# Performance work log

Measured on AMD Instinct MI355X. Metric: run time of the kernel, lower is better.

The kernel has to match this reference:

```python
import jax, jax.numpy as jnp
import numpy as np

B, N, K = 4, 512, 10
PI_SCALE = 0.05  # keeps sum_k pi in (0, 0.5) so the [1e-8, 1] clamp does not saturate at 1
MCMC_KEY = jax.random.key(42)


def setup_inputs() -> dict:
    key = jax.random.key(0)
    k1, k2, k3, k4 = jax.random.split(key, 4)
    mu = jax.random.normal(k1, (B, N, K), dtype=jnp.float32)
    sig = jax.random.uniform(k2, (B, N, K), dtype=jnp.float32)
    pi = jax.random.uniform(k3, (B, N, K), dtype=jnp.float32) * PI_SCALE
    A_0 = jax.random.uniform(k4, (N, N), dtype=jnp.float32)
    return {"mu": mu, "sig": sig, "pi": pi, "A_0": A_0, "num_samples": 100}


def reference(mu, sig, pi, A_0, num_samples):
    b, n, k = mu.shape

    # Mixture-weighted proposal mean/std:  sum_k softmax(pi)_k * {mu,sig}_k
    component_probs = jax.nn.softmax(pi, axis=-1)          # [B,N,K]
    selected_mu = jnp.sum(component_probs * mu, axis=-1)    # [B,N]
    selected_sig = jnp.sum(component_probs * sig, axis=-1)  # [B,N]

    # edge_probs[b,i,j] = clamp(sum_k pi[b,i,k]) -- constant in j; hoisted out of the loop
    # since it depends only on pi (the torch code recomputes it every step).
    edge_probs = jnp.clip(jnp.sum(pi, axis=2), 1e-8, 1.0)[:, :, None]  # [B,N,1]
    log_ep = jnp.log(edge_probs)                                        # [B,N,1]
    log_1mep = jnp.log(1.0 - edge_probs)                                # [B,N,1]

    def log_likelihood(A):  # A: [B,N,N] -> [N]  (sum over dims 0,1 as in torch)
        return jnp.sum(A * log_ep + (1.0 - A) * log_1mep, axis=(0, 1))

    def step(carry, t):
        current_A, acc = carry
        kk = jax.random.fold_in(MCMC_KEY, t)
        k_noise, k_unif = jax.random.split(kk)
        noise = jax.random.normal(k_noise, (b, n), dtype=selected_mu.dtype)
        proposed_mu = selected_mu + noise * selected_sig              # [B,N]
        # sigmoid of rank-1 outer product: einsum('bnc,bmc->bnm') with c==1
        proposed_A = jax.nn.sigmoid(proposed_mu[:, :, None] * proposed_mu[:, None, :])
        ratio = jnp.mean(jnp.clip(jnp.exp(log_likelihood(proposed_A) - log_likelihood(current_A)), 0.0, 1.0))
        accept = jax.random.uniform(k_unif, (b,)) < ratio             # [B] bool
        current_A = jnp.where(accept[:, None, None], proposed_A, current_A)
        return (current_A, acc + current_A), None

    cur0 = jnp.broadcast_to(A_0, (b, n, n)).astype(mu.dtype)
    acc0 = jnp.zeros((b, n, n), dtype=mu.dtype)
    (_, acc), _ = jax.lax.scan(step, (cur0, acc0), jnp.arange(num_samples))
    return acc / num_samples
```

## Files before the change

### kernel.cpp

```cpp
#include <hip/hip_runtime.h>
#include <stdint.h>

#define T_STEPS 100
#define BB 4
#define NN 512
#define KK 10
#define TBTOT (T_STEPS * BB)
#define LLT_ELT ((size_t)TBTOT * NN)

typedef float f4 __attribute__((ext_vector_type(4)));

__device__ __forceinline__ uint32_t rotl32(uint32_t v, int d) {
  return (v << d) | (v >> (32 - d));
}

__device__ __forceinline__ void tf2x32(uint32_t k0, uint32_t k1,
                                       uint32_t& x0, uint32_t& x1) {
  uint32_t k2 = k0 ^ k1 ^ 0x1BD11BDAu;
  x0 += k0; x1 += k1;
#define TFR(r) { x0 += x1; x1 = rotl32(x1, r); x1 ^= x0; }
  TFR(13) TFR(15) TFR(26) TFR(6)   x0 += k1; x1 += k2 + 1u;
  TFR(17) TFR(29) TFR(16) TFR(24)  x0 += k2; x1 += k0 + 2u;
  TFR(13) TFR(15) TFR(26) TFR(6)   x0 += k0; x1 += k1 + 3u;
  TFR(17) TFR(29) TFR(16) TFR(24)  x0 += k1; x1 += k2 + 4u;
  TFR(13) TFR(15) TFR(26) TFR(6)   x0 += k2; x1 += k0 + 5u;
#undef TFR
}

__device__ __forceinline__ float bits_to_u01(uint32_t bits) {
  return __fsub_rn(__uint_as_float((bits >> 9) | 0x3f800000u), 1.0f);
}

__device__ __forceinline__ float erfinv_f32(float x) {
  float w = -logf(__fmul_rn(__fsub_rn(1.0f, x), __fadd_rn(1.0f, x)));
  float p;
  if (w < 5.0f) {
    w = __fsub_rn(w, 2.5f);
    p = 2.81022636e-08f;
    p = __fadd_rn(__fmul_rn(p, w), 3.43273939e-07f);
    p = __fadd_rn(__fmul_rn(p, w), -3.5233877e-06f);
    p = __fadd_rn(__fmul_rn(p, w), -4.39150654e-06f);
    p = __fadd_rn(__fmul_rn(p, w), 0.00021858087f);
    p = __fadd_rn(__fmul_rn(p, w), -0.00125372503f);
    p = __fadd_rn(__fmul_rn(p, w), -0.00417768164f);
    p = __fadd_rn(__fmul_rn(p, w), 0.246640727f);
    p = __fadd_rn(__fmul_rn(p, w), 1.50140941f);
  } else {
    w = __fsub_rn(sqrtf(w), 3.0f);
    p = -0.000200214257f;
    p = __fadd_rn(__fmul_rn(p, w), 0.000100950558f);
    p = __fadd_rn(__fmul_rn(p, w), 0.00134934322f);
    p = __fadd_rn(__fmul_rn(p, w), -0.00367342844f);
    p = __fadd_rn(__fmul_rn(p, w), 0.00573950773f);
    p = __fadd_rn(__fmul_rn(p, w), -0.0076224613f);
    p = __fadd_rn(__fmul_rn(p, w), 0.00943887047f);
    p = __fadd_rn(__fmul_rn(p, w), 1.00167406f);
    p = __fadd_rn(__fmul_rn(p, w), 2.83297682f);
  }
  return __fmul_rn(p, x);
}

__device__ __forceinline__ float fast_sigmoid(float x) {
  float e = __expf(-x);
  return __builtin_amdgcn_rcpf(__fadd_rn(1.0f, e));
}

template <int CTRL>
__device__ __forceinline__ float dpp_add(float x) {
  int v = __builtin_amdgcn_update_dpp(0, __float_as_int(x), CTRL, 0xF, 0xF, true);
  return __fadd_rn(x, __int_as_float(v));
}
__device__ __forceinline__ float readlane_f(float x, int lane) {
  return __int_as_float(__builtin_amdgcn_readlane(__float_as_int(x), lane));
}

__global__ void prep_kernel(const float* __restrict__ mu,
                            const float* __restrict__ sig,
                            const float* __restrict__ pi,
                            float* __restrict__ sm, float* __restrict__ ss,
                            float* __restrict__ Lf) {
  int m = blockIdx.x * blockDim.x + threadIdx.x;
  if (m >= BB * NN) return;
  const float* pp = pi + m * KK;
  float mx = pp[0];
  for (int k = 1; k < KK; k++) mx = fmaxf(mx, pp[k]);
  float e[KK]; float s = 0.0f;
  for (int k = 0; k < KK; k++) { e[k] = expf(__fsub_rn(pp[k], mx)); s = __fadd_rn(s, e[k]); }
  float smv = 0.0f, ssv = 0.0f, eps = 0.0f;
  for (int k = 0; k < KK; k++) {
    float p = e[k] / s;
    smv = __fadd_rn(smv, __fmul_rn(p, mu[m * KK + k]));
    ssv = __fadd_rn(ssv, __fmul_rn(p, sig[m * KK + k]));
    eps = __fadd_rn(eps, pp[k]);
  }
  sm[m] = smv; ss[m] = ssv;
  float ep = fminf(fmaxf(eps, 1e-8f), 1.0f);
  float lep = logf(ep);
  float l1 = logf(__fsub_rn(1.0f, ep));
  Lf[m] = (float)((double)lep - (double)l1);
}

__global__ void rng_kernel(const float* __restrict__ sm,
                           const float* __restrict__ ss,
                           float* __restrict__ pm, float* __restrict__ uacc) {
  int id = blockIdx.x * blockDim.x + threadIdx.x;
  if (id >= T_STEPS * BB * NN) return;
  int t = id >> 11;
  int m = id & 2047;

  uint32_t kk0 = 0u, kk1 = (uint32_t)t;
  tf2x32(0u, 42u, kk0, kk1);
  uint32_t n0 = 0u, n1 = 0u; tf2x32(kk0, kk1, n0, n1);
  uint32_t y0 = 0u, y1 = (uint32_t)m;
  tf2x32(n0, n1, y0, y1);
  uint32_t bits = y0 ^ y1;

  float u01 = bits_to_u01(bits);
  const float lo = -0.99999994f;
  float u = fmaxf(lo, __fadd_rn(__fmul_rn(u01, 2.0f), lo));
  float z = __fmul_rn(1.41421356237309515f, erfinv_f32(u));
  pm[id] = __fadd_rn(sm[m], __fmul_rn(z, ss[m]));

  if (m < 4) {
    uint32_t u0 = 0u, u1 = 1u; tf2x32(kk0, kk1, u0, u1);
    uint32_t c0 = 0u, c1 = (uint32_t)m;
    tf2x32(u0, u1, c0, c1);
    uacc[t * 4 + m] = bits_to_u01(c0 ^ c1);
  }
}

template <int SPLIT>
__global__ __launch_bounds__(512) void ll_kernel(const float* __restrict__ pm,
                                                 const float* __restrict__ Lf,
                                                 const float* __restrict__ A0,
                                                 float* __restrict__ llt_p,
                                                 float* __restrict__ ll0_p) {
  constexpr int CH = NN / SPLIT;
  __shared__ float spm[CH];
  __shared__ float sLc[CH];
  int j = threadIdx.x;
  int bi = blockIdx.x;
  if (bi < TBTOT * SPLIT) {
    int tb = bi / SPLIT;
    int s = bi - tb * SPLIT;
    int b = tb & 3;
    int i0 = s * CH;
    if (j < CH) {
      spm[j] = pm[tb * NN + i0 + j];
      sLc[j] = Lf[b * NN + i0 + j];
    }
    float pmj = pm[tb * NN + j];
    __syncthreads();
    double acc = 0.0;
    #pragma unroll 8
    for (int i = 0; i < CH; i += 2) {
      float x0 = __fmul_rn(spm[i], pmj);
      float x1 = __fmul_rn(spm[i + 1], pmj);
      float t0 = __fmul_rn(fast_sigmoid(x0), sLc[i]);
      float t1 = __fmul_rn(fast_sigmoid(x1), sLc[i + 1]);
      acc += (double)__fadd_rn(t0, t1);
    }
    llt_p[(size_t)s * LLT_ELT + (size_t)tb * NN + j] = (float)acc;
  } else {
    int bi2 = bi - TBTOT * SPLIT;
    int b = bi2 / SPLIT;
    int s = bi2 - b * SPLIT;
    int i0 = s * CH;
    if (j < CH) sLc[j] = Lf[b * NN + i0 + j];
    __syncthreads();
    double acc = 0.0;
    #pragma unroll 4
    for (int i = 0; i < CH; i++) {
      acc += (double)A0[(size_t)(i0 + i) * NN + j] * (double)sLc[i];
    }
    ll0_p[s * (BB * NN) + b * NN + j] = (float)acc;
  }
}

template <int SPLIT>
__global__ __launch_bounds__(512) void combine_kernel(const float* __restrict__ llt_p,
                                                      const float* __restrict__ ll0_p,
                                                      float* __restrict__ llt,
                                                      float* __restrict__ ll0) {
  int bi = blockIdx.x;
  int j = threadIdx.x;
  if (bi < T_STEPS) {
    #pragma unroll
    for (int b = 0; b < BB; b++) {
      size_t idx = ((size_t)bi * BB + b) * NN + j;
      double a = (double)llt_p[idx];
      #pragma unroll
      for (int s = 1; s < SPLIT; s++) a += (double)llt_p[(size_t)s * LLT_ELT + idx];
      llt[idx] = (float)a;
    }
  } else {
    #pragma unroll
    for (int b = 0; b < BB; b++) {
      int idx = b * NN + j;
      double a = (double)ll0_p[idx];
      #pragma unroll
      for (int s = 1; s < SPLIT; s++) a += (double)ll0_p[s * (BB * NN) + idx];
      ll0[idx] = (float)a;
    }
  }
}

#define CH_LOADF(BUF, T)                                                     \
  {                                                                          \
    _Pragma("unroll")                                                        \
    for (int b = 0; b < 4; b++) {                                            \
      _Pragma("unroll")                                                      \
      for (int k = 0; k < 2; k++)                                            \
        BUF[b][k] = llt4[(((size_t)(T) * 4 + b) * 2 + k) * 64 + g];          \
    }                                                                        \
  }

#define CH_ACCF(BUF, B)                                                      \
  {                                                                          \
    _Pragma("unroll")                                                        \
    for (int k = 0; k < 2; k++) {                                            \
      _Pragma("unroll")                                                      \
      for (int c = 0; c < 4; c++)                                            \
        C[k][c] += (double)BUF[B][k][c] - (double)cur[B][k][c];              \
      cur[B][k] = BUF[B][k];                                                 \
    }                                                                        \
  }

#define CH_STEPF(BUF, T)                                                     \
  {                                                                          \
    float4 ua = sua[T];                                                      \
    float ps = 0.0f;                                                         \
    _Pragma("unroll")                                                        \
    for (int k = 0; k < 2; k++) {                                            \
      _Pragma("unroll")                                                      \
      for (int c = 0; c < 4; c++) {                                          \
        double ts = ((double)BUF[0][k][c] + (double)BUF[1][k][c]) +          \
                    ((double)BUF[2][k][c] + (double)BUF[3][k][c]);           \
        float e = fminf(__expf((float)(ts - C[k][c])), 1.0f);                \
        ps = __fadd_rn(ps, e);                                               \
      }                                                                      \
    }                                                                        \
    ps = dpp_add<0xB1>(ps);                 \
    ps = dpp_add<0x4E>(ps);                 \
    ps = dpp_add<0x141>(ps);        \
    ps = dpp_add<0x140>(ps);        \
    float s0 = readlane_f(ps, 0), s1 = readlane_f(ps, 16);                   \
    float s2 = readlane_f(ps, 32), s3 = readlane_f(ps, 48);                  \
    float tot = __fadd_rn(__fadd_rn(s0, s1), __fadd_rn(s2, s3));             \
    float ratio = __fmul_rn(tot, 1.0f / 512.0f);                             \
    if (ua.x < ratio) { st.x = (T); CH_ACCF(BUF, 0) }                        \
    if (ua.y < ratio) { st.y = (T); CH_ACCF(BUF, 1) }                        \
    if (ua.z < ratio) { st.z = (T); CH_ACCF(BUF, 2) }                        \
    if (ua.w < ratio) { st.w = (T); CH_ACCF(BUF, 3) }                        \
    if (g == 0) sst[T] = st;                                                 \
  }

__global__ __launch_bounds__(64) void chain_kernel(const float* __restrict__ llt,
                                                   const float* __restrict__ ll0,
                                                   const float* __restrict__ uacc,
                                                   int* __restrict__ counts) {
  __shared__ float4 sua[T_STEPS];
  __shared__ int4 sst[T_STEPS];
  __shared__ int scnt[BB * (T_STEPS + 1)];
  int g = threadIdx.x;

  const float4* uacc4 = (const float4*)uacc;
  for (int t = g; t < T_STEPS; t += 64) sua[t] = uacc4[t];

  const f4* llt4 = (const f4*)llt;
  const f4* ll04 = (const f4*)ll0;

  f4 cur[4][2];
  #pragma unroll
  for (int b = 0; b < 4; b++)
    #pragma unroll
    for (int k = 0; k < 2; k++) cur[b][k] = ll04[(b * 2 + k) * 64 + g];
  double C[2][4];
  #pragma unroll
  for (int k = 0; k < 2; k++)
    #pragma unroll
    for (int c = 0; c < 4; c++)
      C[k][c] = ((double)cur[0][k][c] + (double)cur[1][k][c]) +
                ((double)cur[2][k][c] + (double)cur[3][k][c]);
  int4 st = make_int4(-1, -1, -1, -1);

  f4 R0[4][2], R1[4][2], R2[4][2];
  CH_LOADF(R0, 0)
  CH_LOADF(R1, 1)
  CH_LOADF(R2, 2)
  __syncthreads();

  for (int t = 0; t < 99; t += 3) {
    CH_STEPF(R0, t)
    CH_LOADF(R0, t + 3)
    CH_STEPF(R1, t + 1)
    if (t + 4 < T_STEPS) CH_LOADF(R1, t + 4)
    CH_STEPF(R2, t + 2)
    if (t + 5 < T_STEPS) CH_LOADF(R2, t + 5)
  }
  CH_STEPF(R0, 99)

  __syncthreads();
  for (int s = g; s < BB * (T_STEPS + 1); s += 64) scnt[s] = 0;
  __syncthreads();
  for (int t = g; t < T_STEPS; t += 64) {
    int4 s4 = sst[t];
    atomicAdd(&scnt[0 * (T_STEPS + 1) + s4.x + 1], 1);
    atomicAdd(&scnt[1 * (T_STEPS + 1) + s4.y + 1], 1);
    atomicAdd(&scnt[2 * (T_STEPS + 1) + s4.z + 1], 1);
    atomicAdd(&scnt[3 * (T_STEPS + 1) + s4.w + 1], 1);
  }
  __syncthreads();
  for (int s = g; s < BB * (T_STEPS + 1); s += 64) counts[s] = scnt[s];
}

__global__ __launch_bounds__(512) void out_kernel(const float* __restrict__ pm,
                                                  const float* __restrict__ A0,
                                                  const int* __restrict__ counts,
                                                  float* __restrict__ out) {
  __shared__ int scnt[T_STEPS + 1];
  int b = blockIdx.x >> 9;
  int i = blockIdx.x & 511;
  int j = threadIdx.x;
  if (j < T_STEPS + 1) scnt[j] = counts[b * (T_STEPS + 1) + j];
  __syncthreads();
  float r = (float)scnt[0] * A0[(size_t)i * NN + j];
  #pragma unroll 4
  for (int t = 0; t < T_STEPS; t++) {
    int c = scnt[t + 1];
    if (c) {
      float x = __fmul_rn(pm[(size_t)(t * BB + b) * NN + i],
                          pm[(size_t)(t * BB + b) * NN + j]);
      r += (float)c * fast_sigmoid(x);
    }
  }
  out[((size_t)b * NN + i) * NN + j] = r * 0.01f;
}

extern "C" void kernel_launch(void* const* d_in, const int* in_sizes, int n_in,
                              void* d_out, int out_size, void* d_ws, size_t ws_size,
                              hipStream_t stream) {
  const float* mu  = (const float*)d_in[0];
  const float* sig = (const float*)d_in[1];
  const float* pi  = (const float*)d_in[2];
  const float* A0  = (const float*)d_in[3];

  char* ws = (char*)d_ws;
  size_t off = 0;
  auto alloc = [&](size_t bytes) -> char* {
    char* p = ws + off;
    off += (bytes + 255) & ~(size_t)255;
    return p;
  };
  float* llt  = (float*)alloc(LLT_ELT * 4);
  float* ll0  = (float*)alloc(BB * NN * 4);
  float* pm   = (float*)alloc(LLT_ELT * 4);
  float* Lf   = (float*)alloc(BB * NN * 4);
  float* sm   = (float*)alloc(BB * NN * 4);
  float* ssv  = (float*)alloc(BB * NN * 4);
  float* uacc = (float*)alloc(T_STEPS * 4 * 4);
  int*   cnts = (int*)alloc(BB * (T_STEPS + 1) * 4);
  size_t fixed_end = off;
  float* outp = (float*)d_out;

  size_t part4 = 4 * LLT_ELT * 4 + 4 * BB * NN * 4 + 1024;
  size_t part2 = 2 * LLT_ELT * 4 + 2 * BB * NN * 4 + 1024;
  int split = (ws_size >= fixed_end + part4) ? 4
            : (ws_size >= fixed_end + part2) ? 2 : 1;

  float* llt_p;
  float* ll0_p;
  if (split > 1) {
    llt_p = (float*)alloc((size_t)split * LLT_ELT * 4);
    ll0_p = (float*)alloc((size_t)split * BB * NN * 4);
  } else {
    llt_p = llt;
    ll0_p = ll0;
  }

  prep_kernel<<<8, 256, 0, stream>>>(mu, sig, pi, sm, ssv, Lf);
  rng_kernel<<<(T_STEPS * BB * NN + 255) / 256, 256, 0, stream>>>(sm, ssv, pm, uacc);
  if (split == 4) {
    ll_kernel<4><<<(TBTOT + BB) * 4, 512, 0, stream>>>(pm, Lf, A0, llt_p, ll0_p);
    combine_kernel<4><<<T_STEPS + 1, 512, 0, stream>>>(llt_p, ll0_p, llt, ll0);
  } else if (split == 2) {
    ll_kernel<2><<<(TBTOT + BB) * 2, 512, 0, stream>>>(pm, Lf, A0, llt_p, ll0_p);
    combine_kernel<2><<<T_STEPS + 1, 512, 0, stream>>>(llt_p, ll0_p, llt, ll0);
  } else {
    ll_kernel<1><<<TBTOT + BB, 512, 0, stream>>>(pm, Lf, A0, llt_p, ll0_p);
  }
  chain_kernel<<<1, 64, 0, stream>>>(llt, ll0, uacc, cnts);
  out_kernel<<<BB * NN, 512, 0, stream>>>(pm, A0, cnts, outp);
}
```

Measured before the change: 147.8 us.

## Stream chain log-likelihood chunks through an LDS ring with async global-to-LDS loads

Replaces the three-register-buffer prefetch in the serial chain kernel with a five-slot LDS ring filled by global_load_lds DMA, issued four steps ahead and gated by explicit vmcnt waits. The aim is to hide global memory latency on the single-wave sequential MCMC chain, which issues loads one step ahead and is latency-bound. It adds LDS reads per step, and correctness depends on the hand-counted vmcnt values and on LDS write visibility without a barrier inside a single wave. It also removes the g==0 guard on the sst store.

```diff
diff --git a/kernel.cpp b/kernel.cpp
--- a/kernel.cpp
+++ b/kernel.cpp
@@ -205,28 +205,43 @@
   }
 }
 
-#define CH_LOADF(BUF, T)                                                     \
+#define SLOTS 5
+#define CHUNK_F 2048
+
+#define WAITV(n) { asm volatile("s_waitcnt vmcnt(" #n ")" ::: "memory"); \
+                   __builtin_amdgcn_sched_barrier(0); }
+
+__device__ __forceinline__ void issue_chunk(const float* __restrict__ llt,
+                                            float* lds_slot, int T, int g) {
+  #pragma unroll
+  for (int v = 0; v < 8; v++) {
+    const float* src = llt + ((size_t)T * 8 + v) * 256 + g * 4;
+    float* dst = lds_slot + v * 256;
+    __builtin_amdgcn_global_load_lds(
+        (const __attribute__((address_space(1))) void*)src,
+        (__attribute__((address_space(3))) void*)dst, 16, 0, 0);
+  }
+}
+
+#define CH_READ(BUF, SLOT)                                                   \
   {                                                                          \
     _Pragma("unroll")                                                        \
-    for (int b = 0; b < 4; b++) {                                            \
-      _Pragma("unroll")                                                      \
-      for (int k = 0; k < 2; k++)                                            \
-        BUF[b][k] = llt4[(((size_t)(T) * 4 + b) * 2 + k) * 64 + g];          \
-    }                                                                        \
-  }
-
-#define CH_ACCF(BUF, B)                                                      \
+    for (int v = 0; v < 8; v++)                                              \
+      BUF[v] = *(const f4*)&lring[SLOT][v * 256 + 4 * g];                    \
+  }
+
+#define CH_ACC2(BUF, B)                                                      \
   {                                                                          \
     _Pragma("unroll")                                                        \
     for (int k = 0; k < 2; k++) {                                            \
       _Pragma("unroll")                                                      \
       for (int c = 0; c < 4; c++)                                            \
-        C[k][c] += (double)BUF[B][k][c] - (double)cur[B][k][c];              \
-      cur[B][k] = BUF[B][k];                                                 \
+        C[k][c] += (double)BUF[B * 2 + k][c] - (double)cur[B][k][c];         \
+      cur[B][k] = BUF[B * 2 + k];                                            \
     }                                                                        \
   }
 
-#define CH_STEPF(BUF, T)                                                     \
+#define CH_STEP2(BUF, T)                                                     \
   {                                                                          \
     float4 ua = sua[T];                                                      \
     float ps = 0.0f;                                                         \
@@ -234,31 +249,32 @@
     for (int k = 0; k < 2; k++) {                                            \
       _Pragma("unroll")                                                      \
       for (int c = 0; c < 4; c++) {                                          \
-        double ts = ((double)BUF[0][k][c] + (double)BUF[1][k][c]) +          \
-                    ((double)BUF[2][k][c] + (double)BUF[3][k][c]);           \
+        double ts = ((double)BUF[0 * 2 + k][c] + (double)BUF[1 * 2 + k][c]) +\
+                    ((double)BUF[2 * 2 + k][c] + (double)BUF[3 * 2 + k][c]); \
         float e = fminf(__expf((float)(ts - C[k][c])), 1.0f);                \
         ps = __fadd_rn(ps, e);                                               \
       }                                                                      \
     }                                                                        \
-    ps = dpp_add<0xB1>(ps);                 \
-    ps = dpp_add<0x4E>(ps);                 \
-    ps = dpp_add<0x141>(ps);        \
-    ps = dpp_add<0x140>(ps);        \
+    ps = dpp_add<0xB1>(ps);                                        \
+    ps = dpp_add<0x4E>(ps);                                        \
+    ps = dpp_add<0x141>(ps);                                \
+    ps = dpp_add<0x140>(ps);                                     \
     float s0 = readlane_f(ps, 0), s1 = readlane_f(ps, 16);                   \
     float s2 = readlane_f(ps, 32), s3 = readlane_f(ps, 48);                  \
     float tot = __fadd_rn(__fadd_rn(s0, s1), __fadd_rn(s2, s3));             \
     float ratio = __fmul_rn(tot, 1.0f / 512.0f);                             \
-    if (ua.x < ratio) { st.x = (T); CH_ACCF(BUF, 0) }                        \
-    if (ua.y < ratio) { st.y = (T); CH_ACCF(BUF, 1) }                        \
-    if (ua.z < ratio) { st.z = (T); CH_ACCF(BUF, 2) }                        \
-    if (ua.w < ratio) { st.w = (T); CH_ACCF(BUF, 3) }                        \
-    if (g == 0) sst[T] = st;                                                 \
+    if (ua.x < ratio) { st.x = (T); CH_ACC2(BUF, 0) }                        \
+    if (ua.y < ratio) { st.y = (T); CH_ACC2(BUF, 1) }                        \
+    if (ua.z < ratio) { st.z = (T); CH_ACC2(BUF, 2) }                        \
+    if (ua.w < ratio) { st.w = (T); CH_ACC2(BUF, 3) }                        \
+    sst[T] = st;                                                             \
   }
 
 __global__ __launch_bounds__(64) void chain_kernel(const float* __restrict__ llt,
                                                    const float* __restrict__ ll0,
                                                    const float* __restrict__ uacc,
                                                    int* __restrict__ counts) {
+  __shared__ float lring[SLOTS][CHUNK_F];
   __shared__ float4 sua[T_STEPS];
   __shared__ int4 sst[T_STEPS];
   __shared__ int scnt[BB * (T_STEPS + 1)];
@@ -267,9 +283,7 @@
   const float4* uacc4 = (const float4*)uacc;
   for (int t = g; t < T_STEPS; t += 64) sua[t] = uacc4[t];
 
-  const f4* llt4 = (const f4*)llt;
   const f4* ll04 = (const f4*)ll0;
-
   f4 cur[4][2];
   #pragma unroll
   for (int b = 0; b < 4; b++)
@@ -283,22 +297,25 @@
       C[k][c] = ((double)cur[0][k][c] + (double)cur[1][k][c]) +
                 ((double)cur[2][k][c] + (double)cur[3][k][c]);
   int4 st = make_int4(-1, -1, -1, -1);
-
-  f4 R0[4][2], R1[4][2], R2[4][2];
-  CH_LOADF(R0, 0)
-  CH_LOADF(R1, 1)
-  CH_LOADF(R2, 2)
-  __syncthreads();
-
-  for (int t = 0; t < 99; t += 3) {
-    CH_STEPF(R0, t)
-    CH_LOADF(R0, t + 3)
-    CH_STEPF(R1, t + 1)
-    if (t + 4 < T_STEPS) CH_LOADF(R1, t + 4)
-    CH_STEPF(R2, t + 2)
-    if (t + 5 < T_STEPS) CH_LOADF(R2, t + 5)
-  }
-  CH_STEPF(R0, 99)
+  asm volatile("s_waitcnt vmcnt(0)" ::: "memory");
+
+  issue_chunk(llt, &lring[0][0], 0, g);
+  issue_chunk(llt, &lring[1][0], 1, g);
+  issue_chunk(llt, &lring[2][0], 2, g);
+  issue_chunk(llt, &lring[3][0], 3, g);
+
+  f4 B[8];
+  for (int t = 0; t < 96; t++) {
+    WAITV(24)
+    int slot = t % SLOTS;
+    CH_READ(B, slot)
+    issue_chunk(llt, &lring[(t + 4) % SLOTS][0], t + 4, g);
+    CH_STEP2(B, t)
+  }
+  { WAITV(24) CH_READ(B, 96 % SLOTS) CH_STEP2(B, 96) }
+  { WAITV(16) CH_READ(B, 97 % SLOTS) CH_STEP2(B, 97) }
+  { WAITV(8)  CH_READ(B, 98 % SLOTS) CH_STEP2(B, 98) }
+  { WAITV(0)  CH_READ(B, 99 % SLOTS) CH_STEP2(B, 99) }
 
   __syncthreads();
   for (int s = g; s < BB * (T_STEPS + 1); s += 64) scnt[s] = 0;
```

Result: slower. 151.8 us (+2.7%).
